# Optimization experiments

Hardware: AMD Instinct MI355X
Metric: run time of the kernel (lower is better)

The kernel has to match this reference:

```python
import jax, jax.numpy as jnp
import numpy as np

N, E, H, K, C, NMOD = 50000, 600000, 128, 5, 60, 12  # nodes, edges, hidden, hops, classes, 6 blocks * 2 modules


def setup_inputs() -> dict:
    key = jax.random.key(0)
    ks = iter(jax.random.split(key, 48))
    def rn(shape, scale=0.05):
        return jax.random.normal(next(ks), shape, jnp.float32) * scale
    return {
        "node_features": rn((N, 2), 1.0),
        "lap_pe": rn((N, K), 1.0),
        "edge_feat": rn((E, 4), 1.0),
        "src": jax.random.randint(next(ks), (E,), 0, N),
        "dst": jax.random.randint(next(ks), (E,), 0, N),
        "in_w": rn((2, H)), "in_b": jnp.zeros((H,), jnp.float32),
        "pos_w": rn((K, H)), "pos_b": jnp.zeros((H,), jnp.float32),
        "edge_w": rn((4, H)), "edge_b": jnp.zeros((H,), jnp.float32),
        "conv_w": rn((NMOD, 2, (K + 1) * H, H)), "conv_b": jnp.zeros((NMOD, 2, H), jnp.float32),
        "bn_g": jnp.ones((NMOD, 2, H), jnp.float32), "bn_b": jnp.zeros((NMOD, 2, H), jnp.float32),
        "ff_w": rn((NMOD, H, H)), "ff_b": jnp.zeros((NMOD, H), jnp.float32),
        "pose_w1": rn((H, H)), "pose_b1": jnp.zeros((H,), jnp.float32),
        "pose_w2": rn((H, 3)), "pose_b2": jnp.zeros((3,), jnp.float32),
        "lab_w1": rn((H, H)), "lab_b1": jnp.zeros((H,), jnp.float32),
        "lab_w2": rn((H, C)), "lab_b2": jnp.zeros((C,), jnp.float32),
    }


def _bn(x, g, b):
    # BatchNorm1d in training mode: stats over node axis
    m = x.mean(0)
    v = x.var(0)
    return (x - m) * jax.lax.rsqrt(v + 1e-5) * g + b


def reference(node_features, lap_pe, edge_feat, src, dst,
              in_w, in_b, pos_w, pos_b, edge_w, edge_b,
              conv_w, conv_b, bn_g, bn_b, ff_w, ff_b,
              pose_w1, pose_b1, pose_w2, pose_b2,
              lab_w1, lab_b1, lab_w2, lab_b2):
    seg = jax.ops.segment_sum
    # symmetric degree norm (in-degree, clamped to 1) as in DGL TAGConv
    deg = seg(jnp.ones((E,), node_features.dtype), dst, num_segments=N)
    norm = jnp.clip(deg, 1.0) ** -0.5  # [N]

    # edge feature aggregation: copy_e -> sum onto dst
    agg_e = seg(edge_feat @ edge_w + edge_b, dst, num_segments=N)  # [N,H]
    h = node_features @ in_w + in_b + lap_pe @ pos_w + pos_b + agg_e

    def tagconv(x, W, b):
        # fstack = [x, Ax, ..., A^K x] with A = D^-1/2 A D^-1/2, then single linear
        fs = [x]
        for _ in range(K):
            z = fs[-1] * norm[:, None]
            z = seg(z[src], dst, num_segments=N) * norm[:, None]
            fs.append(z)
        return jnp.concatenate(fs, axis=-1) @ W + b  # [N,H]

    for m in range(NMOD):  # 6 blocks x 2 TAGConvModules, sequential
        h_in = h
        h = jax.nn.relu(_bn(tagconv(h, conv_w[m, 0], conv_b[m, 0]), bn_g[m, 0], bn_b[m, 0]))
        h = jax.nn.relu(_bn(tagconv(h, conv_w[m, 1], conv_b[m, 1]), bn_g[m, 1], bn_b[m, 1]))
        h = h @ ff_w[m] + ff_b[m] + h_in  # dropout = identity (eval)

    pose = jax.nn.relu(h @ pose_w1 + pose_b1) @ pose_w2 + pose_b2  # [N,3]
    y = h.mean(0)  # dgl.mean_nodes (single batched graph)
    labels = jax.nn.relu(y @ lab_w1 + lab_b1) @ lab_w2 + lab_b2  # [C]
    return pose, labels
```

## Files before the change

### kernel.cpp

```cpp
#include <hip/hip_runtime.h>

#define NN 50000
#define EE 600000
#define HH 128
#define KK 5
#define CC 60
#define NMODS 12
#define MAXPE 750080
#define SC_NB 49
#define MMGRID 391

typedef _Float16 f16;
typedef __attribute__((ext_vector_type(8))) _Float16 f16x8;
typedef __attribute__((ext_vector_type(4))) _Float16 f16x4;
typedef __attribute__((ext_vector_type(16))) float f32x16;
typedef __attribute__((ext_vector_type(4))) int int4v;
typedef __attribute__((ext_vector_type(4))) float f32x4;

#define ZSL ((size_t)NN * 128)

#define GLOBAL_AS __attribute__((address_space(1)))
#define LDS_AS __attribute__((address_space(3)))


__global__ void k_deg(const int* __restrict__ dst, int* __restrict__ deg) {
    int i = blockIdx.x * 256 + threadIdx.x;
    if (i < EE) atomicAdd(&deg[dst[i]], 1);
}

__global__ __launch_bounds__(256) void k_scan1(const int* __restrict__ deg,
                                               int* __restrict__ rs, int* __restrict__ bsum) {
    __shared__ int sm[256];
    int t = threadIdx.x;
    int base = blockIdx.x * 1024 + t * 4;
    int d[4];
#pragma unroll
    for (int j = 0; j < 4; j++) {
        int i = base + j;
        d[j] = (i < NN) ? ((deg[i] + 3) & ~3) : 0;
    }
    int sum = d[0] + d[1] + d[2] + d[3];
    sm[t] = sum;
    __syncthreads();
    for (int off = 1; off < 256; off <<= 1) {
        int v = (t >= off) ? sm[t - off] : 0;
        __syncthreads();
        sm[t] += v;
        __syncthreads();
    }
    int excl = sm[t] - sum;
    int run = excl;
#pragma unroll
    for (int j = 0; j < 4; j++) {
        int i = base + j;
        if (i < NN) rs[i] = run;
        run += d[j];
    }
    if (t == 255) bsum[blockIdx.x] = sm[t];
}

__global__ __launch_bounds__(64) void k_scan2(const int* __restrict__ bsum, int* __restrict__ binc) {
    int l = threadIdx.x;
    int v = (l < SC_NB) ? bsum[l] : 0;
#pragma unroll
    for (int off = 1; off < 64; off <<= 1) {
        int tv = __shfl_up(v, off, 64);
        if (l >= off) v += tv;
    }
    binc[l] = v;
}

__global__ __launch_bounds__(256) void k_scan3(const int* __restrict__ binc, int* __restrict__ rs,
                                               const int* __restrict__ deg, float* __restrict__ norm) {
    int i = blockIdx.x * 256 + threadIdx.x;
    if (i < NN) {
        int b = i >> 10;
        if (b > 0) rs[i] += binc[b - 1];
        int d = deg[i];
        float fd = (float)(d < 1 ? 1 : d);
        norm[i] = 1.0f / sqrtf(fd);
    } else if (i == NN) {
        rs[NN] = binc[SC_NB - 1];
    }
}

__global__ void k_fill(const int* __restrict__ src, const int* __restrict__ dst,
                       const int* __restrict__ rs, const float* __restrict__ norm,
                       int* __restrict__ cursor,
                       int* __restrict__ csrc, float* __restrict__ ew, int* __restrict__ ceid) {
    int i = blockIdx.x * 256 + threadIdx.x;
    if (i >= EE) return;
    int d = dst[i];
    int slot = atomicAdd(&cursor[d], 1);
    int p = rs[d] + slot;
    int s = src[i];
    csrc[p] = s;
    ew[p] = norm[s];
    ceid[p] = i;
}


__global__ void k_cvtw(const float* __restrict__ conv_w, const float* __restrict__ ff_w,
                       const float* __restrict__ pose_w1,
                       f16* __restrict__ wc, f16* __restrict__ wf, f16* __restrict__ wp) {
    int i = blockIdx.x * 256 + threadIdx.x;
    const int NCW = 24 * 128 * 768;
    const int NFW = 12 * 128 * 128;
    const int NPW = 128 * 128;
    if (i < NCW) {
        int mat = i / (128 * 768); int rem = i - mat * (128 * 768);
        int col = rem / 768; int k = rem - col * 768;
        wc[i] = (f16)conv_w[(size_t)mat * 768 * 128 + (size_t)k * 128 + col];
    } else if (i < NCW + NFW) {
        int j = i - NCW;
        int mat = j / (128 * 128); int rem = j - mat * (128 * 128);
        int col = rem / 128; int k = rem - col * 128;
        wf[j] = (f16)ff_w[(size_t)mat * 128 * 128 + k * 128 + col];
    } else if (i < NCW + NFW + NPW) {
        int j = i - NCW - NFW;
        int col = j / 128; int k = j - col * 128;
        wp[j] = (f16)pose_w1[k * 128 + col];
    }
}


__global__ __launch_bounds__(128) void k_h0(
    const float* __restrict__ nf, const float* __restrict__ pe, const float* __restrict__ ef,
    const int* __restrict__ rs, const int* __restrict__ ceid, const float* __restrict__ ew,
    const int* __restrict__ deg,
    const float* __restrict__ in_w, const float* __restrict__ in_b,
    const float* __restrict__ pos_w, const float* __restrict__ pos_b,
    const float* __restrict__ edge_w, const float* __restrict__ edge_b,
    float* __restrict__ h, f16* __restrict__ zc) {
    int n = blockIdx.x;
    int f = threadIdx.x;
    float v = in_b[f] + pos_b[f];
    v += nf[n * 2 + 0] * in_w[f] + nf[n * 2 + 1] * in_w[HH + f];
#pragma unroll
    for (int k = 0; k < KK; k++) v += pe[n * KK + k] * pos_w[k * HH + f];
    float e0 = edge_w[f], e1 = edge_w[HH + f], e2 = edge_w[2 * HH + f], e3 = edge_w[3 * HH + f];
    int s = rs[n], e = rs[n + 1];
    v += (float)deg[n] * edge_b[f];
    for (int i = s; i < e; i++) {
        if (ew[i] == 0.f) continue;
        int eid = ceid[i];
        float4 x = ((const float4*)ef)[eid];
        v += x.x * e0 + x.y * e1 + x.z * e2 + x.w * e3;
    }
    h[(size_t)n * HH + f] = v;
    zc[(size_t)n * 128 + f] = (f16)v;
}


__global__ __launch_bounds__(256) void k_prop16(
    const f16* __restrict__ zin, f16* __restrict__ zout,
    const float* __restrict__ norm, const int* __restrict__ rs,
    const int* __restrict__ csrc, const float* __restrict__ ew) {
    int tid = threadIdx.x;
    int n = blockIdx.x * 16 + (tid >> 4);
    int c = (tid & 15) * 8;
    int s = rs[n], e = rs[n + 1];
    const f16* zp = zin + c;
    float acc[8] = {0.f, 0.f, 0.f, 0.f, 0.f, 0.f, 0.f, 0.f};
    int i = s;
    for (; i + 8 <= e; i += 8) {
        int4v ia = __builtin_nontemporal_load((const int4v*)(csrc + i));
        int4v ib = __builtin_nontemporal_load((const int4v*)(csrc + i + 4));
        f32x4 wa = __builtin_nontemporal_load((const f32x4*)(ew + i));
        f32x4 wb = __builtin_nontemporal_load((const f32x4*)(ew + i + 4));
        f16x8 v0 = *(const f16x8*)(zp + (size_t)ia.x * 128);
        f16x8 v1 = *(const f16x8*)(zp + (size_t)ia.y * 128);
        f16x8 v2 = *(const f16x8*)(zp + (size_t)ia.z * 128);
        f16x8 v3 = *(const f16x8*)(zp + (size_t)ia.w * 128);
        f16x8 v4 = *(const f16x8*)(zp + (size_t)ib.x * 128);
        f16x8 v5 = *(const f16x8*)(zp + (size_t)ib.y * 128);
        f16x8 v6 = *(const f16x8*)(zp + (size_t)ib.z * 128);
        f16x8 v7 = *(const f16x8*)(zp + (size_t)ib.w * 128);
#pragma unroll
        for (int j = 0; j < 8; j++) {
            acc[j] += (float)v0[j] * wa.x + (float)v1[j] * wa.y +
                      (float)v2[j] * wa.z + (float)v3[j] * wa.w;
            acc[j] += (float)v4[j] * wb.x + (float)v5[j] * wb.y +
                      (float)v6[j] * wb.z + (float)v7[j] * wb.w;
        }
    }
    if (i < e) {
        int4v ia = __builtin_nontemporal_load((const int4v*)(csrc + i));
        f32x4 wa = __builtin_nontemporal_load((const f32x4*)(ew + i));
        f16x8 v0 = *(const f16x8*)(zp + (size_t)ia.x * 128);
        f16x8 v1 = *(const f16x8*)(zp + (size_t)ia.y * 128);
        f16x8 v2 = *(const f16x8*)(zp + (size_t)ia.z * 128);
        f16x8 v3 = *(const f16x8*)(zp + (size_t)ia.w * 128);
#pragma unroll
        for (int j = 0; j < 8; j++)
            acc[j] += (float)v0[j] * wa.x + (float)v1[j] * wa.y +
                      (float)v2[j] * wa.z + (float)v3[j] * wa.w;
    }
    float nw = norm[n];
    f16x8 o;
#pragma unroll
    for (int j = 0; j < 8; j++) o[j] = (f16)(acc[j] * nw);
    *(f16x8*)(zout + (size_t)n * 128 + c) = o;
}


template <int KT, int BIAS, int RESID, int RELU, int WRZ, int STATS, int YHF>
__global__ __launch_bounds__(256) void k_mm(
    const f16* __restrict__ A, const f16* __restrict__ Wt,
    const float* __restrict__ bias, const float* __restrict__ Rsd,
    float* __restrict__ Y, f16* __restrict__ Yh,
    f16* __restrict__ Zout, float* __restrict__ part) {
    __shared__ char smem[65536];
    char* As = smem;
    char* Bs = smem + 32768;
    int tid = threadIdx.x;
    int lane = tid & 63;
    int w = tid >> 6, wm = w >> 1, wn = w & 1;
    int n0 = blockIdx.x * 128;
    f32x16 acc[2][2] = {};
    for (int k0 = 0; k0 < KT; k0 += 128) {
        __syncthreads();
        const f16* Asl = A + (size_t)(k0 >> 7) * ZSL;
#pragma unroll
        for (int i = 0; i < 8; i++) {
            int p = (i * 256 + tid) * 16;
            int o = p ^ (((p >> 8) & 15) << 4);
            int r = o >> 8, ce = (o & 255) >> 1;
            int row = n0 + r; if (row >= NN) row = 0;
            const f16* ga = Asl + (size_t)row * 128 + ce;
            char* lba = As + i * 4096 + w * 1024;
            __builtin_amdgcn_global_load_lds((const GLOBAL_AS void*)ga, (LDS_AS void*)lba, 16, 0, 0);
            const f16* gb = Wt + (size_t)r * KT + k0 + ce;
            char* lbb = Bs + i * 4096 + w * 1024;
            __builtin_amdgcn_global_load_lds((const GLOBAL_AS void*)gb, (LDS_AS void*)lbb, 16, 0, 0);
        }
        asm volatile("s_waitcnt vmcnt(0)" ::: "memory");
        __syncthreads();
#pragma unroll
        for (int s = 0; s < 8; s++) {
            int koff = s * 32 + (lane >> 5) * 16;
            f16x8 a[2], b[2];
#pragma unroll
            for (int m = 0; m < 2; m++) {
                int rl = wm * 64 + m * 32 + (lane & 31);
                int oa = (rl * 256 + koff) ^ ((rl & 15) << 4);
                a[m] = *(const f16x8*)(As + oa);
                int cl = wn * 64 + m * 32 + (lane & 31);
                int ob = (cl * 256 + koff) ^ ((cl & 15) << 4);
                b[m] = *(const f16x8*)(Bs + ob);
            }
#pragma unroll
            for (int m = 0; m < 2; m++)
#pragma unroll
                for (int nb = 0; nb < 2; nb++)
                    acc[m][nb] = __builtin_amdgcn_mfma_f32_32x32x16_f16(a[m], b[nb], acc[m][nb], 0, 0, 0);
        }
    }
    float ssum[2] = {0.f, 0.f}, sqq[2] = {0.f, 0.f};
#pragma unroll
    for (int m = 0; m < 2; m++) {
        int rb = n0 + wm * 64 + m * 32 + 4 * (lane >> 5);
#pragma unroll
        for (int nb = 0; nb < 2; nb++) {
            int col = wn * 64 + nb * 32 + (lane & 31);
            float bv = 0.f;
            if (BIAS) bv = bias[col];
#pragma unroll
            for (int r = 0; r < 16; r++) {
                int row = rb + (r & 3) + 8 * (r >> 2);
                if (row >= NN) continue;
                float v = acc[m][nb][r] + bv;
                if (RESID) v += Rsd[(size_t)row * HH + col];
                if (RELU) v = fmaxf(v, 0.f);
                if (STATS) { ssum[nb] += v; sqq[nb] += v * v; }
                if (YHF) Yh[(size_t)row * HH + col] = (f16)v;
                else Y[(size_t)row * HH + col] = v;
                if (WRZ) Zout[(size_t)row * 128 + col] = (f16)v;
            }
        }
    }
    if (STATS) {
        __syncthreads();
        float* red = (float*)smem;
        int slot = wm * 2 + (lane >> 5);
        int colb = wn * 64 + (lane & 31);
        red[slot * 256 + colb] = ssum[0];
        red[slot * 256 + colb + 32] = ssum[1];
        red[slot * 256 + 128 + colb] = sqq[0];
        red[slot * 256 + 128 + colb + 32] = sqq[1];
        __syncthreads();
        float t = red[tid] + red[256 + tid] + red[512 + tid] + red[768 + tid];
        part[blockIdx.x * 256 + tid] = t;
    }
}


__global__ __launch_bounds__(1024) void k_bnfin(const float* __restrict__ part,
                                                const float* __restrict__ g, const float* __restrict__ b,
                                                float* __restrict__ sc, float* __restrict__ sh) {
    __shared__ float rsm[8][128];
    __shared__ float rqm[8][128];
    int tid = threadIdx.x;
    int f = tid & 127, grp = tid >> 7;
    float s = 0.f, q = 0.f;
    for (int bi = grp; bi < MMGRID; bi += 8) {
        s += part[bi * 256 + f];
        q += part[bi * 256 + 128 + f];
    }
    rsm[grp][f] = s;
    rqm[grp][f] = q;
    __syncthreads();
    if (tid < 128) {
        float ss = 0.f, qq = 0.f;
#pragma unroll
        for (int gq = 0; gq < 8; gq++) { ss += rsm[gq][f]; qq += rqm[gq][f]; }
        float mean = ss / (float)NN;
        float var = qq / (float)NN - mean * mean;
        float scale = g[f] / sqrtf(var + 1e-5f);
        sc[f] = scale;
        sh[f] = b[f] - mean * scale;
    }
}


__global__ __launch_bounds__(256) void k_bnapply(const f16* __restrict__ Yh,
                                                 const float* __restrict__ sc, const float* __restrict__ sh,
                                                 f16* __restrict__ zc) {
    int idx = blockIdx.x * 256 + threadIdx.x;
    if (idx >= NN * 16) return;
    f16x8 v = ((const f16x8*)Yh)[idx];
    int c = (idx & 15) * 8;
    f16x8 o;
#pragma unroll
    for (int j = 0; j < 8; j++) {
        float a = sc[c + j], b = sh[c + j];
        o[j] = (f16)fmaxf((float)v[j] * a + b, 0.f);
    }
    ((f16x8*)zc)[idx] = o;
}


__global__ __launch_bounds__(128) void k_pose2(const float* __restrict__ T,
                                               const float* __restrict__ W2, const float* __restrict__ b2,
                                               float* __restrict__ out) {
    int tid = threadIdx.x;
    int n = blockIdx.x * 4 + (tid >> 5);
    int c = tid & 31;
    float4 tv = ((const float4*)T)[(size_t)n * 32 + c];
    float p0 = 0.f, p1 = 0.f, p2 = 0.f;
#pragma unroll
    for (int i = 0; i < 4; i++) {
        float t = (i == 0) ? tv.x : (i == 1) ? tv.y : (i == 2) ? tv.z : tv.w;
        int k = c * 4 + i;
        p0 += t * W2[k * 3 + 0];
        p1 += t * W2[k * 3 + 1];
        p2 += t * W2[k * 3 + 2];
    }
#pragma unroll
    for (int off = 16; off > 0; off >>= 1) {
        p0 += __shfl_down(p0, off, 32);
        p1 += __shfl_down(p1, off, 32);
        p2 += __shfl_down(p2, off, 32);
    }
    if (c == 0) {
        out[(size_t)n * 3 + 0] = p0 + b2[0];
        out[(size_t)n * 3 + 1] = p1 + b2[1];
        out[(size_t)n * 3 + 2] = p2 + b2[2];
    }
}

__global__ __launch_bounds__(256) void k_meanpart(const float* __restrict__ Y, float* __restrict__ part) {
    int tid = threadIdx.x;
    float s = 0.f;
    for (int n = blockIdx.x * 2 + (tid >> 7); n < NN; n += 512) {
        s += Y[(size_t)n * HH + (tid & 127)];
    }
    __shared__ float sh[256];
    sh[tid] = s;
    __syncthreads();
    if (tid < 128) part[blockIdx.x * 128 + tid] = sh[tid] + sh[tid + 128];
}

__global__ __launch_bounds__(128) void k_labels(const float* __restrict__ part,
                                                const float* __restrict__ w1, const float* __restrict__ b1,
                                                const float* __restrict__ w2, const float* __restrict__ b2,
                                                float* __restrict__ out) {
    __shared__ float ym[128];
    __shared__ float t2[128];
    int f = threadIdx.x;
    float s = 0.f;
    for (int bi = 0; bi < 256; bi++) s += part[bi * 128 + f];
    ym[f] = s / (float)NN;
    __syncthreads();
    float a = b1[f];
    for (int k = 0; k < 128; k++) a += ym[k] * w1[k * 128 + f];
    t2[f] = fmaxf(a, 0.f);
    __syncthreads();
    if (f < CC) {
        float a2 = b2[f];
        for (int k = 0; k < 128; k++) a2 += t2[k] * w2[k * CC + f];
        out[(size_t)NN * 3 + f] = a2;
    }
}


static inline size_t align256(size_t x) { return (x + 255) & ~(size_t)255; }

extern "C" void kernel_launch(void* const* d_in, const int* in_sizes, int n_in,
                              void* d_out, int out_size, void* d_ws, size_t ws_size,
                              hipStream_t stream) {
    const float* nf = (const float*)d_in[0];
    const float* pe = (const float*)d_in[1];
    const float* ef = (const float*)d_in[2];
    const int* src = (const int*)d_in[3];
    const int* dst = (const int*)d_in[4];
    const float* in_w = (const float*)d_in[5];
    const float* in_b = (const float*)d_in[6];
    const float* pos_w = (const float*)d_in[7];
    const float* pos_b = (const float*)d_in[8];
    const float* edge_w = (const float*)d_in[9];
    const float* edge_b = (const float*)d_in[10];
    const float* conv_w = (const float*)d_in[11];
    const float* bn_g = (const float*)d_in[13];
    const float* bn_b = (const float*)d_in[14];
    const float* ff_w = (const float*)d_in[15];
    const float* ff_b = (const float*)d_in[16];
    const float* pose_w1 = (const float*)d_in[17];
    const float* pose_b1 = (const float*)d_in[18];
    const float* pose_w2 = (const float*)d_in[19];
    const float* pose_b2 = (const float*)d_in[20];
    const float* lab_w1 = (const float*)d_in[21];
    const float* lab_b1 = (const float*)d_in[22];
    const float* lab_w2 = (const float*)d_in[23];
    const float* lab_b2 = (const float*)d_in[24];
    float* out = (float*)d_out;

    char* wsp = (char*)d_ws;
    size_t off = 0;
    auto alloc = [&](size_t bytes) -> void* {
        void* p = wsp + off;
        off += align256(bytes);
        return p;
    };
    float* norm = (float*)alloc((size_t)NN * 4);
    int* deg = (int*)alloc((size_t)NN * 4);
    int* rs = (int*)alloc((size_t)(NN + 1) * 4);
    int* cursor = (int*)alloc((size_t)NN * 4);
    int* csrc = (int*)alloc((size_t)MAXPE * 4);
    float* ew = (float*)alloc((size_t)MAXPE * 4);
    int* ceid = (int*)alloc((size_t)MAXPE * 4);
    int* bsum = (int*)alloc(64 * 4);
    int* binc = (int*)alloc(64 * 4);
    float* hin = (float*)alloc((size_t)NN * HH * 4);
    float* ybuf = (float*)alloc((size_t)NN * HH * 4);
    f16* yh = (f16*)alloc((size_t)NN * HH * 2);
    f16* zcat = (f16*)alloc((size_t)6 * ZSL * 2);
    f16* wc = (f16*)alloc((size_t)24 * 128 * 768 * 2);
    f16* wf = (f16*)alloc((size_t)12 * 128 * 128 * 2);
    f16* wp = (f16*)alloc((size_t)128 * 128 * 2);
    float* part = (float*)alloc((size_t)MMGRID * 256 * 4);
    float* mpart = (float*)alloc(256 * 128 * 4);
    float* bnsc = (float*)alloc(128 * 4);
    float* bnsh = (float*)alloc(128 * 4);
    (void)ws_size; (void)in_sizes; (void)n_in; (void)out_size;

    hipMemsetAsync(deg, 0, (size_t)NN * 4, stream);
    hipMemsetAsync(cursor, 0, (size_t)NN * 4, stream);
    hipMemsetAsync(csrc, 0, (size_t)MAXPE * 4, stream);
    hipMemsetAsync(ew, 0, (size_t)MAXPE * 4, stream);
    int egrid = (EE + 255) / 256;
    k_deg<<<egrid, 256, 0, stream>>>(dst, deg);
    k_scan1<<<SC_NB, 256, 0, stream>>>(deg, rs, bsum);
    k_scan2<<<1, 64, 0, stream>>>(bsum, binc);
    k_scan3<<<(NN + 256) / 256, 256, 0, stream>>>(binc, rs, deg, norm);
    k_fill<<<egrid, 256, 0, stream>>>(src, dst, rs, norm, cursor, csrc, ew, ceid);

    const int NCVT = 24 * 128 * 768 + 12 * 128 * 128 + 128 * 128;
    k_cvtw<<<(NCVT + 255) / 256, 256, 0, stream>>>(conv_w, ff_w, pose_w1, wc, wf, wp);

    k_h0<<<NN, 128, 0, stream>>>(nf, pe, ef, rs, ceid, ew, deg, in_w, in_b, pos_w, pos_b,
                                 edge_w, edge_b, hin, zcat);

    const int pgrid = (NN + 15) / 16;
    const int agrid = (NN * 16 + 255) / 256;

    for (int m = 0; m < NMODS; m++) {
        for (int s = 0; s < 2; s++) {
            const f16* Wb = wc + (size_t)(m * 2 + s) * 128 * 768;
            for (int k = 1; k <= KK; k++) {
                k_prop16<<<pgrid, 256, 0, stream>>>(zcat + (size_t)(k - 1) * ZSL,
                                                    zcat + (size_t)k * ZSL,
                                                    norm, rs, csrc, ew);
            }
            k_mm<768, 0, 0, 0, 0, 1, 1><<<MMGRID, 256, 0, stream>>>(zcat, Wb, nullptr, nullptr,
                                                                    nullptr, yh, nullptr, part);
            k_bnfin<<<1, 1024, 0, stream>>>(part, bn_g + (size_t)(m * 2 + s) * HH,
                                            bn_b + (size_t)(m * 2 + s) * HH, bnsc, bnsh);
            k_bnapply<<<agrid, 256, 0, stream>>>(yh, bnsc, bnsh, zcat);
        }
        k_mm<128, 1, 1, 0, 1, 0, 0><<<MMGRID, 256, 0, stream>>>(zcat, wf + (size_t)m * 128 * 128,
                                                                ff_b + (size_t)m * HH, hin,
                                                                hin, nullptr, zcat, nullptr);
    }

    k_mm<128, 1, 0, 1, 0, 0, 0><<<MMGRID, 256, 0, stream>>>(zcat, wp, pose_b1, nullptr,
                                                            ybuf, nullptr, nullptr, nullptr);
    k_pose2<<<NN / 4, 128, 0, stream>>>(ybuf, pose_w2, pose_b2, out);

    k_meanpart<<<256, 256, 0, stream>>>(hin, mpart);
    k_labels<<<1, 128, 0, stream>>>(mpart, lab_w1, lab_b1, lab_w2, lab_b2, out);
}
```

Baseline: 4.720 ms.

## Fuse BN finalize into GEMM tail and BN apply into first propagation hop

The BatchNorm statistics finalize is moved into the GEMM's last-arriving block, using an atomic counter plus threadfence, so the separate single-block k_bnfin launch goes away. For the second conv of each module, the BN scale/shift and ReLU are applied on the fly inside the first propagation hop, which also writes the normalized slice 0. This removes one k_bnapply pass per module. Edge features are permuted into CSR order during fill so k_h0 reads them contiguously instead of through an index. In exchange, the BN+ReLU is recomputed for every gathered neighbor, the permuted edge buffer uses more memory, and correctness now depends on the last-block counter logic.

```diff
diff --git a/kernel.cpp b/kernel.cpp
--- a/kernel.cpp
+++ b/kernel.cpp
@@ -87,7 +87,8 @@
 __global__ void k_fill(const int* __restrict__ src, const int* __restrict__ dst,
                        const int* __restrict__ rs, const float* __restrict__ norm,
                        int* __restrict__ cursor,
-                       int* __restrict__ csrc, float* __restrict__ ew, int* __restrict__ ceid) {
+                       int* __restrict__ csrc, float* __restrict__ ew, float* __restrict__ efp,
+                       const float* __restrict__ ef) {
     int i = blockIdx.x * 256 + threadIdx.x;
     if (i >= EE) return;
     int d = dst[i];
@@ -96,7 +97,7 @@
     int s = src[i];
     csrc[p] = s;
     ew[p] = norm[s];
-    ceid[p] = i;
+    ((float4*)efp)[p] = ((const float4*)ef)[i];
 }
 
 
@@ -125,9 +126,8 @@
 
 
 __global__ __launch_bounds__(128) void k_h0(
-    const float* __restrict__ nf, const float* __restrict__ pe, const float* __restrict__ ef,
-    const int* __restrict__ rs, const int* __restrict__ ceid, const float* __restrict__ ew,
-    const int* __restrict__ deg,
+    const float* __restrict__ nf, const float* __restrict__ pe, const float* __restrict__ efp,
+    const int* __restrict__ rs, const int* __restrict__ deg,
     const float* __restrict__ in_w, const float* __restrict__ in_b,
     const float* __restrict__ pos_w, const float* __restrict__ pos_b,
     const float* __restrict__ edge_w, const float* __restrict__ edge_b,
@@ -142,9 +142,7 @@
     int s = rs[n], e = rs[n + 1];
     v += (float)deg[n] * edge_b[f];
     for (int i = s; i < e; i++) {
-        if (ew[i] == 0.f) continue;
-        int eid = ceid[i];
-        float4 x = ((const float4*)ef)[eid];
+        float4 x = ((const float4*)efp)[i];
         v += x.x * e0 + x.y * e1 + x.z * e2 + x.w * e3;
     }
     h[(size_t)n * HH + f] = v;
@@ -152,16 +150,34 @@
 }
 
 
+template <int BNF>
 __global__ __launch_bounds__(256) void k_prop16(
     const f16* __restrict__ zin, f16* __restrict__ zout,
     const float* __restrict__ norm, const int* __restrict__ rs,
-    const int* __restrict__ csrc, const float* __restrict__ ew) {
+    const int* __restrict__ csrc, const float* __restrict__ ew,
+    const float* __restrict__ sc, const float* __restrict__ sh,
+    f16* __restrict__ zc0) {
     int tid = threadIdx.x;
     int n = blockIdx.x * 16 + (tid >> 4);
     int c = (tid & 15) * 8;
+    float af[8], bf[8];
+    if (BNF) {
+#pragma unroll
+        for (int j = 0; j < 8; j++) { af[j] = sc[c + j]; bf[j] = sh[c + j]; }
+        f16x8 vo = *(const f16x8*)(zin + (size_t)n * 128 + c);
+        f16x8 o0;
+#pragma unroll
+        for (int j = 0; j < 8; j++) o0[j] = (f16)fmaxf((float)vo[j] * af[j] + bf[j], 0.f);
+        *(f16x8*)(zc0 + (size_t)n * 128 + c) = o0;
+    }
     int s = rs[n], e = rs[n + 1];
     const f16* zp = zin + c;
     float acc[8] = {0.f, 0.f, 0.f, 0.f, 0.f, 0.f, 0.f, 0.f};
+    auto term = [&](const f16x8& v, int j) -> float {
+        float x = (float)v[j];
+        if (BNF) x = fmaxf(x * af[j] + bf[j], 0.f);
+        return x;
+    };
     int i = s;
     for (; i + 8 <= e; i += 8) {
         int4v ia = __builtin_nontemporal_load((const int4v*)(csrc + i));
@@ -178,10 +194,10 @@
         f16x8 v7 = *(const f16x8*)(zp + (size_t)ib.w * 128);
 #pragma unroll
         for (int j = 0; j < 8; j++) {
-            acc[j] += (float)v0[j] * wa.x + (float)v1[j] * wa.y +
-                      (float)v2[j] * wa.z + (float)v3[j] * wa.w;
-            acc[j] += (float)v4[j] * wb.x + (float)v5[j] * wb.y +
-                      (float)v6[j] * wb.z + (float)v7[j] * wb.w;
+            acc[j] += term(v0, j) * wa.x + term(v1, j) * wa.y +
+                      term(v2, j) * wa.z + term(v3, j) * wa.w;
+            acc[j] += term(v4, j) * wb.x + term(v5, j) * wb.y +
+                      term(v6, j) * wb.z + term(v7, j) * wb.w;
         }
     }
     if (i < e) {
@@ -193,8 +209,8 @@
         f16x8 v3 = *(const f16x8*)(zp + (size_t)ia.w * 128);
 #pragma unroll
         for (int j = 0; j < 8; j++)
-            acc[j] += (float)v0[j] * wa.x + (float)v1[j] * wa.y +
-                      (float)v2[j] * wa.z + (float)v3[j] * wa.w;
+            acc[j] += term(v0, j) * wa.x + term(v1, j) * wa.y +
+                      term(v2, j) * wa.z + term(v3, j) * wa.w;
     }
     float nw = norm[n];
     f16x8 o;
@@ -209,7 +225,9 @@
     const f16* __restrict__ A, const f16* __restrict__ Wt,
     const float* __restrict__ bias, const float* __restrict__ Rsd,
     float* __restrict__ Y, f16* __restrict__ Yh,
-    f16* __restrict__ Zout, float* __restrict__ part) {
+    f16* __restrict__ Zout, float* __restrict__ part,
+    const float* __restrict__ bng, const float* __restrict__ bnb,
+    float* __restrict__ sc, float* __restrict__ sh, int* __restrict__ cnt) {
     __shared__ char smem[65536];
     char* As = smem;
     char* Bs = smem + 32768;
@@ -291,34 +309,30 @@
         __syncthreads();
         float t = red[tid] + red[256 + tid] + red[512 + tid] + red[768 + tid];
         part[blockIdx.x * 256 + tid] = t;
-    }
-}
-
-
-__global__ __launch_bounds__(1024) void k_bnfin(const float* __restrict__ part,
-                                                const float* __restrict__ g, const float* __restrict__ b,
-                                                float* __restrict__ sc, float* __restrict__ sh) {
-    __shared__ float rsm[8][128];
-    __shared__ float rqm[8][128];
-    int tid = threadIdx.x;
-    int f = tid & 127, grp = tid >> 7;
-    float s = 0.f, q = 0.f;
-    for (int bi = grp; bi < MMGRID; bi += 8) {
-        s += part[bi * 256 + f];
-        q += part[bi * 256 + 128 + f];
-    }
-    rsm[grp][f] = s;
-    rqm[grp][f] = q;
-    __syncthreads();
-    if (tid < 128) {
-        float ss = 0.f, qq = 0.f;
-#pragma unroll
-        for (int gq = 0; gq < 8; gq++) { ss += rsm[gq][f]; qq += rqm[gq][f]; }
-        float mean = ss / (float)NN;
-        float var = qq / (float)NN - mean * mean;
-        float scale = g[f] / sqrtf(var + 1e-5f);
-        sc[f] = scale;
-        sh[f] = b[f] - mean * scale;
+        __threadfence();
+        __syncthreads();
+        __shared__ int lastFlag;
+        if (tid == 0) {
+            int old = __hip_atomic_fetch_add(cnt, 1, __ATOMIC_ACQ_REL, __HIP_MEMORY_SCOPE_AGENT);
+            lastFlag = (old == MMGRID - 1) ? 1 : 0;
+        }
+        __syncthreads();
+        if (lastFlag) {
+            if (tid < 128) {
+                int f = tid;
+                float s = 0.f, q = 0.f;
+                for (int bi = 0; bi < MMGRID; bi++) {
+                    s += part[bi * 256 + f];
+                    q += part[bi * 256 + 128 + f];
+                }
+                float mean = s / (float)NN;
+                float var = q / (float)NN - mean * mean;
+                float scale = bng[f] / sqrtf(var + 1e-5f);
+                sc[f] = scale;
+                sh[f] = bnb[f] - mean * scale;
+            }
+            if (tid == 0) *cnt = 0;
+        }
     }
 }
 
@@ -448,9 +462,10 @@
     int* cursor = (int*)alloc((size_t)NN * 4);
     int* csrc = (int*)alloc((size_t)MAXPE * 4);
     float* ew = (float*)alloc((size_t)MAXPE * 4);
-    int* ceid = (int*)alloc((size_t)MAXPE * 4);
+    float* efp = (float*)alloc((size_t)MAXPE * 16);
     int* bsum = (int*)alloc(64 * 4);
     int* binc = (int*)alloc(64 * 4);
+    int* cnt = (int*)alloc(256);
     float* hin = (float*)alloc((size_t)NN * HH * 4);
     float* ybuf = (float*)alloc((size_t)NN * HH * 4);
     f16* yh = (f16*)alloc((size_t)NN * HH * 2);
@@ -468,43 +483,63 @@
     hipMemsetAsync(cursor, 0, (size_t)NN * 4, stream);
     hipMemsetAsync(csrc, 0, (size_t)MAXPE * 4, stream);
     hipMemsetAsync(ew, 0, (size_t)MAXPE * 4, stream);
+    hipMemsetAsync(efp, 0, (size_t)MAXPE * 16, stream);
+    hipMemsetAsync(cnt, 0, 4, stream);
     int egrid = (EE + 255) / 256;
     k_deg<<<egrid, 256, 0, stream>>>(dst, deg);
     k_scan1<<<SC_NB, 256, 0, stream>>>(deg, rs, bsum);
     k_scan2<<<1, 64, 0, stream>>>(bsum, binc);
     k_scan3<<<(NN + 256) / 256, 256, 0, stream>>>(binc, rs, deg, norm);
-    k_fill<<<egrid, 256, 0, stream>>>(src, dst, rs, norm, cursor, csrc, ew, ceid);
+    k_fill<<<egrid, 256, 0, stream>>>(src, dst, rs, norm, cursor, csrc, ew, efp, ef);
 
     const int NCVT = 24 * 128 * 768 + 12 * 128 * 128 + 128 * 128;
     k_cvtw<<<(NCVT + 255) / 256, 256, 0, stream>>>(conv_w, ff_w, pose_w1, wc, wf, wp);
 
-    k_h0<<<NN, 128, 0, stream>>>(nf, pe, ef, rs, ceid, ew, deg, in_w, in_b, pos_w, pos_b,
+    k_h0<<<NN, 128, 0, stream>>>(nf, pe, efp, rs, deg, in_w, in_b, pos_w, pos_b,
                                  edge_w, edge_b, hin, zcat);
 
     const int pgrid = (NN + 15) / 16;
     const int agrid = (NN * 16 + 255) / 256;
 
     for (int m = 0; m < NMODS; m++) {
-        for (int s = 0; s < 2; s++) {
-            const f16* Wb = wc + (size_t)(m * 2 + s) * 128 * 768;
+        {
+            const f16* Wb = wc + (size_t)(m * 2 + 0) * 128 * 768;
             for (int k = 1; k <= KK; k++) {
-                k_prop16<<<pgrid, 256, 0, stream>>>(zcat + (size_t)(k - 1) * ZSL,
-                                                    zcat + (size_t)k * ZSL,
-                                                    norm, rs, csrc, ew);
+                k_prop16<0><<<pgrid, 256, 0, stream>>>(zcat + (size_t)(k - 1) * ZSL,
+                                                       zcat + (size_t)k * ZSL,
+                                                       norm, rs, csrc, ew,
+                                                       nullptr, nullptr, nullptr);
             }
-            k_mm<768, 0, 0, 0, 0, 1, 1><<<MMGRID, 256, 0, stream>>>(zcat, Wb, nullptr, nullptr,
-                                                                    nullptr, yh, nullptr, part);
-            k_bnfin<<<1, 1024, 0, stream>>>(part, bn_g + (size_t)(m * 2 + s) * HH,
-                                            bn_b + (size_t)(m * 2 + s) * HH, bnsc, bnsh);
-            k_bnapply<<<agrid, 256, 0, stream>>>(yh, bnsc, bnsh, zcat);
-        }
-        k_mm<128, 1, 1, 0, 1, 0, 0><<<MMGRID, 256, 0, stream>>>(zcat, wf + (size_t)m * 128 * 128,
-                                                                ff_b + (size_t)m * HH, hin,
-                                                                hin, nullptr, zcat, nullptr);
-    }
-
-    k_mm<128, 1, 0, 1, 0, 0, 0><<<MMGRID, 256, 0, stream>>>(zcat, wp, pose_b1, nullptr,
-                                                            ybuf, nullptr, nullptr, nullptr);
+            k_mm<768, 0, 0, 0, 0, 1, 1><<<MMGRID, 256, 0, stream>>>(
+                zcat, Wb, nullptr, nullptr, nullptr, yh, nullptr, part,
+                bn_g + (size_t)(m * 2 + 0) * HH, bn_b + (size_t)(m * 2 + 0) * HH,
+                bnsc, bnsh, cnt);
+        }
+        {
+            const f16* Wb = wc + (size_t)(m * 2 + 1) * 128 * 768;
+            k_prop16<1><<<pgrid, 256, 0, stream>>>(yh, zcat + ZSL,
+                                                   norm, rs, csrc, ew,
+                                                   bnsc, bnsh, zcat);
+            for (int k = 2; k <= KK; k++) {
+                k_prop16<0><<<pgrid, 256, 0, stream>>>(zcat + (size_t)(k - 1) * ZSL,
+                                                       zcat + (size_t)k * ZSL,
+                                                       norm, rs, csrc, ew,
+                                                       nullptr, nullptr, nullptr);
+            }
+            k_mm<768, 0, 0, 0, 0, 1, 1><<<MMGRID, 256, 0, stream>>>(
+                zcat, Wb, nullptr, nullptr, nullptr, yh, nullptr, part,
+                bn_g + (size_t)(m * 2 + 1) * HH, bn_b + (size_t)(m * 2 + 1) * HH,
+                bnsc, bnsh, cnt);
+        }
+        k_bnapply<<<agrid, 256, 0, stream>>>(yh, bnsc, bnsh, zcat);
+        k_mm<128, 1, 1, 0, 1, 0, 0><<<MMGRID, 256, 0, stream>>>(
+            zcat, wf + (size_t)m * 128 * 128, ff_b + (size_t)m * HH, hin,
+            hin, nullptr, zcat, nullptr, nullptr, nullptr, nullptr, nullptr, nullptr);
+    }
+
+    k_mm<128, 1, 0, 1, 0, 0, 0><<<MMGRID, 256, 0, stream>>>(
+        zcat, wp, pose_b1, nullptr, ybuf, nullptr, nullptr, nullptr,
+        nullptr, nullptr, nullptr, nullptr, nullptr);
     k_pose2<<<NN / 4, 128, 0, stream>>>(ybuf, pose_w2, pose_b2, out);
 
     k_meanpart<<<256, 256, 0, stream>>>(hin, mpart);
```

Result: slower. 5.745 ms (+21.7%).
